# Optimization experiments

Hardware: AMD Instinct MI355X
Metric: run time of the kernel (lower is better)

Reference implementation:

```python
import jax, jax.numpy as jnp
import numpy as np

N, E, C = 50000, 800000, 100000
D_IN, HID = 128, 128
MLP_IN, MLP_HID = 2 * HID + 1, HID // 2
BN_EPS = 1e-5
NEG_SLOPE = 0.01


def setup_inputs() -> dict:
    key = jax.random.key(0)
    ks = jax.random.split(key, 24)
    inp = {
        "x": jax.random.normal(ks[0], (N, D_IN), jnp.float32),
        "src": jax.random.randint(ks[1], (E,), 0, N, jnp.int32),
        "dst": jax.random.randint(ks[2], (E,), 0, N, jnp.int32),
        "cand_u": jax.random.randint(ks[3], (C,), 0, N, jnp.int32),
        "cand_v": jax.random.randint(ks[4], (C,), 0, N, jnp.int32),
        "cand_feat": jax.random.normal(ks[5], (C, 1), jnp.float32),
    }
    s = 1.0 / np.sqrt(D_IN)
    # SAGEConv layer 0 and 1 (in=out=128 since statedim == pnhid)
    for li, k0 in [(0, 6), (1, 12)]:
        inp[f"w_self{li}"] = jax.random.uniform(ks[k0], (D_IN, HID), jnp.float32, -s, s)
        inp[f"w_neigh{li}"] = jax.random.uniform(ks[k0 + 1], (D_IN, HID), jnp.float32, -s, s)
        inp[f"b{li}"] = jnp.zeros((HID,), jnp.float32)
        inp[f"gamma{li}"] = jnp.ones((HID,), jnp.float32)
        inp[f"beta{li}"] = jnp.zeros((HID,), jnp.float32)
        inp[f"rm{li}"] = jax.random.normal(ks[k0 + 2], (HID,), jnp.float32) * 0.1
        inp[f"rv{li}"] = jax.random.uniform(ks[k0 + 3], (HID,), jnp.float32, 0.5, 1.5)
    # confidence MLP: 257 -> 64 -> 64 -> 1
    sizes = [MLP_IN, MLP_HID, MLP_HID, 1]
    for i in range(3):
        si = 1.0 / np.sqrt(sizes[i])
        inp[f"mw{i}"] = jax.random.uniform(ks[18 + 2 * i], (sizes[i], sizes[i + 1]), jnp.float32, -si, si)
        inp[f"mb{i}"] = jax.random.uniform(ks[19 + 2 * i], (sizes[i + 1],), jnp.float32, -si, si)
    return inp


def _sage_bn_block(x, src, dst, w_self, w_neigh, b, gamma, beta, rm, rv):
    # mean aggregation over incoming edges (gather -> scatter-add -> divide)
    msgs = x[src]  # [E, D]
    agg = jax.ops.segment_sum(msgs, dst, num_segments=N)  # [N, D]
    deg = jax.ops.segment_sum(jnp.ones((src.shape[0],), x.dtype), dst, num_segments=N)
    agg = agg / jnp.maximum(deg, 1.0)[:, None]
    h = x @ w_self + agg @ w_neigh + b
    # BatchNorm1d (eval mode, running stats) then leaky_relu; dropout is identity in eval
    h = gamma * (h - rm) * jax.lax.rsqrt(rv + BN_EPS) + beta
    return jax.nn.leaky_relu(h, NEG_SLOPE)


def reference(x, src, dst, cand_u, cand_v, cand_feat,
              w_self0, w_neigh0, b0, gamma0, beta0, rm0, rv0,
              w_self1, w_neigh1, b1, gamma1, beta1, rm1, rv1,
              mw0, mb0, mw1, mb1, mw2, mb2):
    h = _sage_bn_block(x, src, dst, w_self0, w_neigh0, b0, gamma0, beta0, rm0, rv0)
    h = _sage_bn_block(h, src, dst, w_self1, w_neigh1, b1, gamma1, beta1, rm1, rv1)
    h = jnp.nan_to_num(h, nan=1e-14)
    # candidate embeddings: [C, 2*HID + 1]
    ce = jnp.concatenate([h[cand_u], h[cand_v], cand_feat], axis=-1)
    z = jax.nn.leaky_relu(ce @ mw0 + mb0, NEG_SLOPE)
    z = jax.nn.leaky_relu(z @ mw1 + mb1, NEG_SLOPE)
    y = z @ mw2 + mb2  # [C, 1]
    return y, jax.nn.softmax(y, axis=0)
```

## Files before the change

kernel.cpp:

```cpp
#include <hip/hip_runtime.h>
#include <math.h>

#define N_NODES 50000
#define N_EDGES 800000
#define N_CAND  100000
#define D       128
#define BN_EPS  1e-5f
#define SLOPE   0.01f

#define NB2     196
#define TILE    4096
#define NTILE   196
#define BCAP    4736

typedef __attribute__((ext_vector_type(8))) short bf16x8;
typedef __attribute__((ext_vector_type(4))) float f32x4;

__device__ __forceinline__ float lrelu(float x){ return x >= 0.f ? x : SLOPE * x; }

__device__ __forceinline__ unsigned short f2bf_rn(float f){
  unsigned int u = __float_as_uint(f);
  unsigned int r = u + 0x7FFFu + ((u >> 16) & 1u);
  return (unsigned short)(r >> 16);
}
__device__ __forceinline__ float bf2f(unsigned short h){
  return __uint_as_float(((unsigned int)h) << 16);
}
__device__ __forceinline__ float4 bf4f(ushort4 u){
  return make_float4(__uint_as_float((unsigned)u.x << 16),
                     __uint_as_float((unsigned)u.y << 16),
                     __uint_as_float((unsigned)u.z << 16),
                     __uint_as_float((unsigned)u.w << 16));
}

__global__ __launch_bounds__(256) void k_bin(const int* __restrict__ src, const int* __restrict__ dst,
                                             int* __restrict__ gcnt, unsigned* __restrict__ ebin, int E){
  __shared__ unsigned stage[TILE];
  __shared__ int hist[256], lscan[256], lex[256], lcur[256], gbase[256];
  __shared__ int stot;
  int t = threadIdx.x;
  int e0 = blockIdx.x * TILE;

  hist[t] = 0;
  __syncthreads();

  unsigned pk[16]; int bk[16]; bool ok[16];
  #pragma unroll
  for (int j = 0; j < 16; ++j){
    int i = e0 + j * 256 + t;
    ok[j] = (i < E);
    if (ok[j]){
      int d = dst[i];
      pk[j] = ((unsigned)d << 16) | (unsigned)src[i];
      bk[j] = d >> 8;
      atomicAdd(&hist[bk[j]], 1);
    }
  }
  __syncthreads();

  lscan[t] = hist[t];
  __syncthreads();
  for (int off = 1; off < 256; off <<= 1){
    int v = (t >= off) ? lscan[t - off] : 0;
    __syncthreads();
    lscan[t] += v;
    __syncthreads();
  }
  int ex = lscan[t] - hist[t];
  lex[t]  = ex;
  lcur[t] = ex;
  if (t < NB2) gbase[t] = hist[t] ? atomicAdd(&gcnt[t], hist[t]) : 0;
  if (t == 255) stot = lscan[255];
  __syncthreads();

  #pragma unroll
  for (int j = 0; j < 16; ++j){
    if (ok[j]){
      int p = atomicAdd(&lcur[bk[j]], 1);
      stage[p] = pk[j];
    }
  }
  __syncthreads();

  int tot = stot;
  for (int i = t; i < tot; i += 256){
    unsigned e = stage[i];
    int b = (int)(e >> 24);
    ebin[(size_t)b * BCAP + gbase[b] + (i - lex[b])] = e;
  }
}

__global__ __launch_bounds__(256) void k_bscan2(const int* __restrict__ gcnt, int* __restrict__ bbase,
                                                int* __restrict__ rowptr){
  __shared__ int sd[256];
  int t = threadIdx.x;
  int v = (t < NB2) ? gcnt[t] : 0;
  sd[t] = v; __syncthreads();
  for (int off = 1; off < 256; off <<= 1){
    int a = (t >= off) ? sd[t - off] : 0;
    __syncthreads();
    sd[t] += a; __syncthreads();
  }
  if (t < NB2) bbase[t] = sd[t] - v;
  if (t == NB2 - 1) rowptr[N_NODES] = sd[t];
}

__global__ __launch_bounds__(256) void k_bfin(const int* __restrict__ gcnt, const int* __restrict__ bbase,
                                              const unsigned* __restrict__ ebin,
                                              unsigned short* __restrict__ eid16,
                                              int* __restrict__ rowptr, int n){
  __shared__ int hist[256], lb[256], lcur[256];
  int t = threadIdx.x, b = blockIdx.x;
  int cb   = gcnt[b];
  int base = bbase[b];
  const unsigned* eb = &ebin[(size_t)b * BCAP];
  hist[t] = 0;
  __syncthreads();
  for (int idx = t; idx < cb; idx += 256) atomicAdd(&hist[(eb[idx] >> 16) & 255], 1);
  __syncthreads();
  lb[t] = hist[t];
  __syncthreads();
  for (int off = 1; off < 256; off <<= 1){
    int v = (t >= off) ? lb[t - off] : 0;
    __syncthreads();
    lb[t] += v; __syncthreads();
  }
  int ex = lb[t] - hist[t];
  lcur[t] = ex;
  int node = (b << 8) + t;
  if (node < n) rowptr[node] = base + ex;
  __syncthreads();
  for (int idx = t; idx < cb; idx += 256){
    unsigned e = eb[idx];
    int p = atomicAdd(&lcur[(e >> 16) & 255], 1);
    eid16[base + p] = (unsigned short)(e & 0xffffu);
  }
}

__global__ __launch_bounds__(256) void k_cvt_w(const float* __restrict__ ws, const float* __restrict__ wn,
                                               unsigned short* __restrict__ bth, unsigned short* __restrict__ btl){
  int col = blockIdx.x;
  int k   = threadIdx.x;
  float v = (k < 128) ? ws[k * D + col] : wn[(k - 128) * D + col];
  unsigned short hi = f2bf_rn(v);
  unsigned short lo = f2bf_rn(v - bf2f(hi));
  bth[col * 256 + k] = hi;
  btl[col * 256 + k] = lo;
}

__global__ __launch_bounds__(256) void k_cvt_mlp(const float* __restrict__ w, int K, int Kpad,
                                                 unsigned short* __restrict__ th, unsigned short* __restrict__ tl){
  int col = blockIdx.x;
  for (int k = threadIdx.x; k < Kpad; k += 256){
    float v = (k < K) ? w[k * 64 + col] : 0.f;
    unsigned short hi = f2bf_rn(v);
    th[col * Kpad + k] = hi;
    tl[col * Kpad + k] = f2bf_rn(v - bf2f(hi));
  }
}

__global__ __launch_bounds__(256) void k_cvt_x(const float* __restrict__ X, unsigned short* __restrict__ XB, int nel4){
  int i = blockIdx.x * 256 + threadIdx.x;
  if (i < nel4){
    float4 v = *reinterpret_cast<const float4*>(&X[(size_t)i * 4]);
    ushort4 u;
    u.x = f2bf_rn(v.x); u.y = f2bf_rn(v.y); u.z = f2bf_rn(v.z); u.w = f2bf_rn(v.w);
    *reinterpret_cast<ushort4*>(&XB[(size_t)i * 4]) = u;
  }
}

__global__ __launch_bounds__(256) void k_agg_bf(const unsigned short* __restrict__ XB,
                                                const int* __restrict__ rowptr, const unsigned short* __restrict__ eid,
                                                float* __restrict__ AG, int n){
  int g = blockIdx.x * 8 + (threadIdx.x >> 5);
  int l = threadIdx.x & 31;
  if (g >= n) return;
  int e0 = rowptr[g], e1 = rowptr[g + 1];
  float4 a0 = make_float4(0.f,0.f,0.f,0.f);
  float4 a1 = make_float4(0.f,0.f,0.f,0.f);
  float4 a2 = make_float4(0.f,0.f,0.f,0.f);
  float4 a3 = make_float4(0.f,0.f,0.f,0.f);
  int e = e0;
  for (; e + 4 <= e1; e += 4){
    int s0 = eid[e], s1 = eid[e + 1], s2 = eid[e + 2], s3 = eid[e + 3];
    ushort4 u0 = *reinterpret_cast<const ushort4*>(&XB[(size_t)s0 * D + l * 4]);
    ushort4 u1 = *reinterpret_cast<const ushort4*>(&XB[(size_t)s1 * D + l * 4]);
    ushort4 u2 = *reinterpret_cast<const ushort4*>(&XB[(size_t)s2 * D + l * 4]);
    ushort4 u3 = *reinterpret_cast<const ushort4*>(&XB[(size_t)s3 * D + l * 4]);
    float4 f0 = bf4f(u0), f1 = bf4f(u1), f2 = bf4f(u2), f3 = bf4f(u3);
    a0.x += f0.x; a0.y += f0.y; a0.z += f0.z; a0.w += f0.w;
    a1.x += f1.x; a1.y += f1.y; a1.z += f1.z; a1.w += f1.w;
    a2.x += f2.x; a2.y += f2.y; a2.z += f2.z; a2.w += f2.w;
    a3.x += f3.x; a3.y += f3.y; a3.z += f3.z; a3.w += f3.w;
  }
  for (; e < e1; ++e){
    int s0 = eid[e];
    ushort4 u0 = *reinterpret_cast<const ushort4*>(&XB[(size_t)s0 * D + l * 4]);
    float4 f0 = bf4f(u0);
    a0.x += f0.x; a0.y += f0.y; a0.z += f0.z; a0.w += f0.w;
  }
  float sc = 1.f / fmaxf((float)(e1 - e0), 1.f);
  float4 o;
  o.x = (a0.x + a1.x + a2.x + a3.x) * sc;
  o.y = (a0.y + a1.y + a2.y + a3.y) * sc;
  o.z = (a0.z + a1.z + a2.z + a3.z) * sc;
  o.w = (a0.w + a1.w + a2.w + a3.w) * sc;
  *reinterpret_cast<float4*>(&AG[(size_t)g * D + l * 4]) = o;
}

__global__ __launch_bounds__(256) void k_sage_mfma(const float* __restrict__ XS, const float* __restrict__ AG,
    const unsigned short* __restrict__ BTH, const unsigned short* __restrict__ BTL,
    const float* __restrict__ Bb, const float* __restrict__ GM, const float* __restrict__ BT,
    const float* __restrict__ RM, const float* __restrict__ RV,
    float* __restrict__ H, unsigned short* __restrict__ HBH, unsigned short* __restrict__ HBL,
    int n, int donan)
{
  __shared__ unsigned short Ah[64 * 40];
  __shared__ unsigned short Al[64 * 40];
  __shared__ unsigned short Bh[128 * 40];
  __shared__ unsigned short Bl[128 * 40];

  int t  = threadIdx.x;
  int l  = t & 63;
  int wv = t >> 6;
  int lm = l & 15;
  int lk = l >> 4;
  int node0 = blockIdx.x * 64;

  f32x4 acc[8];
  #pragma unroll
  for (int f = 0; f < 8; ++f) acc[f] = (f32x4){0.f, 0.f, 0.f, 0.f};

  for (int step = 0; step < 8; ++step){
    int k0 = step * 32;
    const float* srcA = (step < 4) ? XS : AG;
    int koff = (step < 4) ? k0 : (k0 - 128);

    __syncthreads();
    #pragma unroll
    for (int i = 0; i < 2; ++i){
      int c   = t + i * 256;
      int row = c >> 3, c4 = c & 7;
      int node = min(node0 + row, n - 1);
      float4 v = *reinterpret_cast<const float4*>(&srcA[(size_t)node * D + koff + c4 * 4]);
      const float* vp = (const float*)&v;
      unsigned short hh[4], ll[4];
      #pragma unroll
      for (int j = 0; j < 4; ++j){
        unsigned short hi = f2bf_rn(vp[j]);
        hh[j] = hi;
        ll[j] = f2bf_rn(vp[j] - bf2f(hi));
      }
      uint2 wh, wl;
      wh.x = (unsigned)hh[0] | ((unsigned)hh[1] << 16);
      wh.y = (unsigned)hh[2] | ((unsigned)hh[3] << 16);
      wl.x = (unsigned)ll[0] | ((unsigned)ll[1] << 16);
      wl.y = (unsigned)ll[2] | ((unsigned)ll[3] << 16);
      *reinterpret_cast<uint2*>(&Ah[row * 40 + c4 * 4]) = wh;
      *reinterpret_cast<uint2*>(&Al[row * 40 + c4 * 4]) = wl;
    }
    #pragma unroll
    for (int i = 0; i < 2; ++i){
      int c   = t + i * 256;
      int col = c >> 2, q = c & 3;
      *reinterpret_cast<uint4*>(&Bh[col * 40 + q * 8]) =
          *reinterpret_cast<const uint4*>(&BTH[col * 256 + k0 + q * 8]);
      *reinterpret_cast<uint4*>(&Bl[col * 40 + q * 8]) =
          *reinterpret_cast<const uint4*>(&BTL[col * 256 + k0 + q * 8]);
    }
    __syncthreads();

    bf16x8 afh = *reinterpret_cast<const bf16x8*>(&Ah[(wv * 16 + lm) * 40 + lk * 8]);
    bf16x8 afl = *reinterpret_cast<const bf16x8*>(&Al[(wv * 16 + lm) * 40 + lk * 8]);
    #pragma unroll
    for (int f = 0; f < 8; ++f){
      bf16x8 bfh = *reinterpret_cast<const bf16x8*>(&Bh[(f * 16 + lm) * 40 + lk * 8]);
      bf16x8 bfl = *reinterpret_cast<const bf16x8*>(&Bl[(f * 16 + lm) * 40 + lk * 8]);
      acc[f] = __builtin_amdgcn_mfma_f32_16x16x32_bf16(afh, bfh, acc[f], 0, 0, 0);
      acc[f] = __builtin_amdgcn_mfma_f32_16x16x32_bf16(afl, bfh, acc[f], 0, 0, 0);
      acc[f] = __builtin_amdgcn_mfma_f32_16x16x32_bf16(afh, bfl, acc[f], 0, 0, 0);
    }
  }

  #pragma unroll
  for (int f = 0; f < 8; ++f){
    int col = f * 16 + lm;
    float s  = GM[col] * rsqrtf(RV[col] + BN_EPS);
    float cj = (Bb[col] - RM[col]) * s + BT[col];
    #pragma unroll
    for (int r = 0; r < 4; ++r){
      int node = node0 + wv * 16 + lk * 4 + r;
      if (node < n){
        float v = lrelu(acc[f][r] * s + cj);
        if (donan && (v != v)) v = 1e-14f;
        if (H)  H[(size_t)node * D + col] = v;
        unsigned short h16 = f2bf_rn(v);
        if (HBH) HBH[(size_t)node * D + col] = h16;
        if (HBL) HBL[(size_t)node * D + col] = f2bf_rn(v - bf2f(h16));
      }
    }
  }
}

__global__ __launch_bounds__(256) void k_mlp_mfma(
    const unsigned short* __restrict__ HH, const unsigned short* __restrict__ HL,
    const int* __restrict__ cu, const int* __restrict__ cv, const float* __restrict__ cf,
    const unsigned short* __restrict__ W0H, const unsigned short* __restrict__ W0L,
    const float* __restrict__ mw0, const float* __restrict__ mb0,
    const unsigned short* __restrict__ W1H, const unsigned short* __restrict__ W1L,
    const float* __restrict__ mb1, const float* __restrict__ mw2, const float* __restrict__ mb2,
    float* __restrict__ y, int C)
{
  __shared__ unsigned short zh[4][32 * 72];
  __shared__ unsigned short zl[4][32 * 72];

  int t = threadIdx.x;
  int wv = t >> 6, l = t & 63, lm = l & 15, lk = l >> 4;
  int candbase = blockIdx.x * 128 + wv * 32;

  int c0 = min(candbase + lm,      C - 1);
  int c1 = min(candbase + 16 + lm, C - 1);
  int nu0 = cu[c0], nv0 = cv[c0];
  int nu1 = cu[c1], nv1 = cv[c1];

  f32x4 acc[2][4];
  #pragma unroll
  for (int m = 0; m < 2; ++m)
    #pragma unroll
    for (int f = 0; f < 4; ++f) acc[m][f] = (f32x4){0.f, 0.f, 0.f, 0.f};

  int kbase = lk * 8;
  bf16x8 ah0 = *reinterpret_cast<const bf16x8*>(&HH[(size_t)nu0 * D + kbase]);
  bf16x8 al0 = *reinterpret_cast<const bf16x8*>(&HL[(size_t)nu0 * D + kbase]);
  bf16x8 ah1 = *reinterpret_cast<const bf16x8*>(&HH[(size_t)nu1 * D + kbase]);
  bf16x8 al1 = *reinterpret_cast<const bf16x8*>(&HL[(size_t)nu1 * D + kbase]);

  #pragma unroll
  for (int s = 0; s < 8; ++s){
    bf16x8 nh0, nl0, nh1, nl1;
    if (s < 7){
      int n0 = (s + 1 < 4) ? nu0 : nv0;
      int n1 = (s + 1 < 4) ? nu1 : nv1;
      int koff = ((s + 1) & 3) * 32 + kbase;
      nh0 = *reinterpret_cast<const bf16x8*>(&HH[(size_t)n0 * D + koff]);
      nl0 = *reinterpret_cast<const bf16x8*>(&HL[(size_t)n0 * D + koff]);
      nh1 = *reinterpret_cast<const bf16x8*>(&HH[(size_t)n1 * D + koff]);
      nl1 = *reinterpret_cast<const bf16x8*>(&HL[(size_t)n1 * D + koff]);
    }
    int k0 = s * 32 + kbase;
    #pragma unroll
    for (int f = 0; f < 4; ++f){
      int col = f * 16 + lm;
      bf16x8 bh = *reinterpret_cast<const bf16x8*>(&W0H[(size_t)col * 264 + k0]);
      bf16x8 bl = *reinterpret_cast<const bf16x8*>(&W0L[(size_t)col * 264 + k0]);
      acc[0][f] = __builtin_amdgcn_mfma_f32_16x16x32_bf16(ah0, bh, acc[0][f], 0, 0, 0);
      acc[0][f] = __builtin_amdgcn_mfma_f32_16x16x32_bf16(al0, bh, acc[0][f], 0, 0, 0);
      acc[0][f] = __builtin_amdgcn_mfma_f32_16x16x32_bf16(ah0, bl, acc[0][f], 0, 0, 0);
      acc[1][f] = __builtin_amdgcn_mfma_f32_16x16x32_bf16(ah1, bh, acc[1][f], 0, 0, 0);
      acc[1][f] = __builtin_amdgcn_mfma_f32_16x16x32_bf16(al1, bh, acc[1][f], 0, 0, 0);
      acc[1][f] = __builtin_amdgcn_mfma_f32_16x16x32_bf16(ah1, bl, acc[1][f], 0, 0, 0);
    }
    if (s < 7){ ah0 = nh0; al0 = nl0; ah1 = nh1; al1 = nl1; }
  }

  float cfv[2][4];
  #pragma unroll
  for (int m = 0; m < 2; ++m)
    #pragma unroll
    for (int r = 0; r < 4; ++r)
      cfv[m][r] = cf[min(candbase + m * 16 + lk * 4 + r, C - 1)];

  #pragma unroll
  for (int f = 0; f < 4; ++f){
    int col = f * 16 + lm;
    float b0v = mb0[col];
    float wfv = mw0[256 * 64 + col];
    #pragma unroll
    for (int m = 0; m < 2; ++m){
      #pragma unroll
      for (int r = 0; r < 4; ++r){
        int cl = m * 16 + lk * 4 + r;
        float z = lrelu(acc[m][f][r] + b0v + cfv[m][r] * wfv);
        unsigned short h16 = f2bf_rn(z);
        zh[wv][cl * 72 + col] = h16;
        zl[wv][cl * 72 + col] = f2bf_rn(z - bf2f(h16));
      }
    }
  }

  f32x4 a2[2][4];
  #pragma unroll
  for (int m = 0; m < 2; ++m)
    #pragma unroll
    for (int f = 0; f < 4; ++f) a2[m][f] = (f32x4){0.f, 0.f, 0.f, 0.f};

  #pragma unroll
  for (int s2 = 0; s2 < 2; ++s2){
    int kk = s2 * 32 + kbase;
    bf16x8 azh0 = *reinterpret_cast<const bf16x8*>(&zh[wv][(0 * 16 + lm) * 72 + kk]);
    bf16x8 azl0 = *reinterpret_cast<const bf16x8*>(&zl[wv][(0 * 16 + lm) * 72 + kk]);
    bf16x8 azh1 = *reinterpret_cast<const bf16x8*>(&zh[wv][(1 * 16 + lm) * 72 + kk]);
    bf16x8 azl1 = *reinterpret_cast<const bf16x8*>(&zl[wv][(1 * 16 + lm) * 72 + kk]);
    #pragma unroll
    for (int f = 0; f < 4; ++f){
      int col = f * 16 + lm;
      bf16x8 bh = *reinterpret_cast<const bf16x8*>(&W1H[(size_t)col * 64 + kk]);
      bf16x8 bl = *reinterpret_cast<const bf16x8*>(&W1L[(size_t)col * 64 + kk]);
      a2[0][f] = __builtin_amdgcn_mfma_f32_16x16x32_bf16(azh0, bh, a2[0][f], 0, 0, 0);
      a2[0][f] = __builtin_amdgcn_mfma_f32_16x16x32_bf16(azl0, bh, a2[0][f], 0, 0, 0);
      a2[0][f] = __builtin_amdgcn_mfma_f32_16x16x32_bf16(azh0, bl, a2[0][f], 0, 0, 0);
      a2[1][f] = __builtin_amdgcn_mfma_f32_16x16x32_bf16(azh1, bh, a2[1][f], 0, 0, 0);
      a2[1][f] = __builtin_amdgcn_mfma_f32_16x16x32_bf16(azl1, bh, a2[1][f], 0, 0, 0);
      a2[1][f] = __builtin_amdgcn_mfma_f32_16x16x32_bf16(azh1, bl, a2[1][f], 0, 0, 0);
    }
  }

  float p00 = 0.f, p01 = 0.f, p02 = 0.f, p03 = 0.f;
  float p10 = 0.f, p11 = 0.f, p12 = 0.f, p13 = 0.f;
  #pragma unroll
  for (int f = 0; f < 4; ++f){
    int col = f * 16 + lm;
    float b1v = mb1[col];
    float w2v = mw2[col];
    p00 = fmaf(lrelu(a2[0][f][0] + b1v), w2v, p00);
    p01 = fmaf(lrelu(a2[0][f][1] + b1v), w2v, p01);
    p02 = fmaf(lrelu(a2[0][f][2] + b1v), w2v, p02);
    p03 = fmaf(lrelu(a2[0][f][3] + b1v), w2v, p03);
    p10 = fmaf(lrelu(a2[1][f][0] + b1v), w2v, p10);
    p11 = fmaf(lrelu(a2[1][f][1] + b1v), w2v, p11);
    p12 = fmaf(lrelu(a2[1][f][2] + b1v), w2v, p12);
    p13 = fmaf(lrelu(a2[1][f][3] + b1v), w2v, p13);
  }
  #pragma unroll
  for (int off = 1; off < 16; off <<= 1){
    p00 += __shfl_xor(p00, off); p01 += __shfl_xor(p01, off);
    p02 += __shfl_xor(p02, off); p03 += __shfl_xor(p03, off);
    p10 += __shfl_xor(p10, off); p11 += __shfl_xor(p11, off);
    p12 += __shfl_xor(p12, off); p13 += __shfl_xor(p13, off);
  }
  if (lm == 0){
    float b2 = mb2[0];
    int base0 = candbase + lk * 4;
    int base1 = candbase + 16 + lk * 4;
    if (base0 + 0 < C) y[base0 + 0] = p00 + b2;
    if (base0 + 1 < C) y[base0 + 1] = p01 + b2;
    if (base0 + 2 < C) y[base0 + 2] = p02 + b2;
    if (base0 + 3 < C) y[base0 + 3] = p03 + b2;
    if (base1 + 0 < C) y[base1 + 0] = p10 + b2;
    if (base1 + 1 < C) y[base1 + 1] = p11 + b2;
    if (base1 + 2 < C) y[base1 + 2] = p12 + b2;
    if (base1 + 3 < C) y[base1 + 3] = p13 + b2;
  }
}

__global__ __launch_bounds__(256) void k_red1(const float* __restrict__ y,
                                              float* __restrict__ bmax, float* __restrict__ bsum, int C){
  __shared__ float sm[4];
  __shared__ float ss[4];
  int t = threadIdx.x;
  float m = -3.4e38f;
  for (int i = blockIdx.x * 256 + t; i < C; i += gridDim.x * 256) m = fmaxf(m, y[i]);
  for (int o = 32; o; o >>= 1) m = fmaxf(m, __shfl_xor(m, o));
  if ((t & 63) == 0) sm[t >> 6] = m;
  __syncthreads();
  float bm = fmaxf(fmaxf(sm[0], sm[1]), fmaxf(sm[2], sm[3]));
  float s = 0.f;
  for (int i = blockIdx.x * 256 + t; i < C; i += gridDim.x * 256) s += expf(y[i] - bm);
  for (int o = 32; o; o >>= 1) s += __shfl_xor(s, o);
  if ((t & 63) == 0) ss[t >> 6] = s;
  __syncthreads();
  if (t == 0){ bmax[blockIdx.x] = bm; bsum[blockIdx.x] = ss[0] + ss[1] + ss[2] + ss[3]; }
}

__global__ __launch_bounds__(256) void k_red2(const float* __restrict__ bmax, const float* __restrict__ bsum,
                                              float* __restrict__ g, int nb){
  __shared__ float sm[4];
  __shared__ float ss[4];
  int t = threadIdx.x;
  float m0 = (t < nb) ? bmax[t] : -3.4e38f;
  float m = m0;
  for (int o = 32; o; o >>= 1) m = fmaxf(m, __shfl_xor(m, o));
  if ((t & 63) == 0) sm[t >> 6] = m;
  __syncthreads();
  float gm = fmaxf(fmaxf(sm[0], sm[1]), fmaxf(sm[2], sm[3]));
  float s = (t < nb) ? bsum[t] * expf(m0 - gm) : 0.f;
  for (int o = 32; o; o >>= 1) s += __shfl_xor(s, o);
  if ((t & 63) == 0) ss[t >> 6] = s;
  __syncthreads();
  if (t == 0){ g[0] = gm; g[1] = 1.f / (ss[0] + ss[1] + ss[2] + ss[3]); }
}

__global__ __launch_bounds__(256) void k_red3(const float* __restrict__ y, const float* __restrict__ g,
                                              float* __restrict__ out, int C){
  int i = blockIdx.x * 256 + threadIdx.x;
  if (i < C) out[i] = expf(y[i] - g[0]) * g[1];
}

extern "C" void kernel_launch(void* const* d_in, const int* in_sizes, int n_in,
                              void* d_out, int out_size, void* d_ws, size_t ws_size,
                              hipStream_t stream)
{
  const float* x   = (const float*)d_in[0];
  const int*   src = (const int*)  d_in[1];
  const int*   dst = (const int*)  d_in[2];
  const int*   cu  = (const int*)  d_in[3];
  const int*   cv  = (const int*)  d_in[4];
  const float* cf  = (const float*)d_in[5];
  const float* ws0 = (const float*)d_in[6];
  const float* wn0 = (const float*)d_in[7];
  const float* b0  = (const float*)d_in[8];
  const float* g0  = (const float*)d_in[9];
  const float* be0 = (const float*)d_in[10];
  const float* rm0 = (const float*)d_in[11];
  const float* rv0 = (const float*)d_in[12];
  const float* ws1 = (const float*)d_in[13];
  const float* wn1 = (const float*)d_in[14];
  const float* b1  = (const float*)d_in[15];
  const float* g1  = (const float*)d_in[16];
  const float* be1 = (const float*)d_in[17];
  const float* rm1 = (const float*)d_in[18];
  const float* rv1 = (const float*)d_in[19];
  const float* mw0 = (const float*)d_in[20];
  const float* mb0 = (const float*)d_in[21];
  const float* mw1 = (const float*)d_in[22];
  const float* mb1 = (const float*)d_in[23];
  const float* mw2 = (const float*)d_in[24];
  const float* mb2 = (const float*)d_in[25];

  float* out = (float*)d_out;

  char* w = (char*)d_ws;
  float* aggn  = (float*)w; w += (size_t)N_NODES * D * 4;
  float* h0    = (float*)w; w += (size_t)N_NODES * D * 4;
  float* h1    = (float*)w; w += (size_t)N_NODES * D * 4;
  int* cnt     = (int*)w;   w += (size_t)N_NODES * 4;
  int* rowptr  = (int*)w;   w += (size_t)(N_NODES + 1) * 4;
  int* cur     = (int*)w;   w += (size_t)N_NODES * 4;
  int* eid     = (int*)w;   w += (size_t)N_EDGES * 4;
  int* gcnt    = (int*)w;   w += (size_t)(NB2 + 8) * 4;
  int* bbase   = (int*)w;   w += (size_t)(NB2 + 1) * 4;
  float* bmax  = (float*)w; w += 256 * 4;
  float* bsumF = (float*)w; w += 256 * 4;
  float* gred  = (float*)w; w += 2 * 4;
  unsigned short* w0th = (unsigned short*)w; w += (size_t)64 * 264 * 2;
  unsigned short* w0tl = (unsigned short*)w; w += (size_t)64 * 264 * 2;
  unsigned short* w1th = (unsigned short*)w; w += (size_t)64 * 64 * 2;
  unsigned short* w1tl = (unsigned short*)w; w += (size_t)64 * 64 * 2;

  unsigned short* eid16 = (unsigned short*)eid;

  unsigned* ebin = (unsigned*)h0;

  unsigned short* xb   = (unsigned short*)h1;
  unsigned short* hb0  = xb + (size_t)N_NODES * D;
  unsigned short* hb1h = (unsigned short*)h1;
  unsigned short* hb1l = hb1h + (size_t)N_NODES * D;

  unsigned short* bth0 = (unsigned short*)cnt;
  unsigned short* btl0 = bth0 + 128 * 256;
  unsigned short* bth1 = (unsigned short*)cur;
  unsigned short* btl1 = bth1 + 128 * 256;

  hipMemsetAsync(gcnt, 0, (size_t)NB2 * 4, stream);
  k_bin   <<<NTILE, 256, 0, stream>>>(src, dst, gcnt, ebin, N_EDGES);
  k_bscan2<<<1, 256, 0, stream>>>(gcnt, bbase, rowptr);
  k_bfin  <<<NB2, 256, 0, stream>>>(gcnt, bbase, ebin, eid16, rowptr, N_NODES);

  k_cvt_w<<<128, 256, 0, stream>>>(ws0, wn0, bth0, btl0);
  k_cvt_w<<<128, 256, 0, stream>>>(ws1, wn1, bth1, btl1);
  k_cvt_mlp<<<64, 256, 0, stream>>>(mw0, 257, 264, w0th, w0tl);
  k_cvt_mlp<<<64, 256, 0, stream>>>(mw1, 64, 64, w1th, w1tl);
  k_cvt_x<<<(N_NODES * D / 4 + 255) / 256, 256, 0, stream>>>(x, xb, N_NODES * D / 4);

  int GB = (N_NODES + 63) / 64;
  k_agg_bf<<<(N_NODES + 7) / 8, 256, 0, stream>>>(xb, rowptr, eid16, aggn, N_NODES);
  k_sage_mfma<<<GB, 256, 0, stream>>>(x,  aggn, bth0, btl0, b0, g0, be0, rm0, rv0,
                                      h0, hb0, (unsigned short*)0, N_NODES, 0);
  k_agg_bf<<<(N_NODES + 7) / 8, 256, 0, stream>>>(hb0, rowptr, eid16, aggn, N_NODES);
  k_sage_mfma<<<GB, 256, 0, stream>>>(h0, aggn, bth1, btl1, b1, g1, be1, rm1, rv1,
                                      (float*)0, hb1h, hb1l, N_NODES, 1);

  k_mlp_mfma<<<(N_CAND + 127) / 128, 256, 0, stream>>>(hb1h, hb1l, cu, cv, cf,
      w0th, w0tl, mw0, mb0, w1th, w1tl, mb1, mw2, mb2, out, N_CAND);

  k_red1<<<256, 256, 0, stream>>>(out, bmax, bsumF, N_CAND);
  k_red2<<<1, 256, 0, stream>>>(bmax, bsumF, gred, 256);
  k_red3<<<(N_CAND + 255) / 256, 256, 0, stream>>>(out, gred, out + N_CAND, N_CAND);
}
```

Baseline: 230.2 us.

## Precompute per-node first MLP layer projections instead of per-candidate GEMM

The first MLP layer is linear in the concatenated node embeddings, so it is split into per-node projections h@W_u and h@W_v, computed once for all 50k nodes by a new GEMM kernel and stored as hi/lo bf16 pairs. The candidate kernel then gathers two 64-wide projected rows per candidate and adds them with bias and the scalar feature term, replacing the 257-deep per-candidate MFMA. This roughly halves the layer-0 FLOPs (50k vs 100k rows) but adds a separate kernel launch and an extra write and read of the projected buffers. Storing the projections as split bf16 adds a small rounding step before the sum.

```diff
diff --git a/kernel.cpp b/kernel.cpp
--- a/kernel.cpp
+++ b/kernel.cpp
@@ -26,11 +26,25 @@
 __device__ __forceinline__ float bf2f(unsigned short h){
   return __uint_as_float(((unsigned int)h) << 16);
 }
+__device__ __forceinline__ float bfu(unsigned u){ return __uint_as_float(u << 16); }
+__device__ __forceinline__ float bfh(unsigned u){ return __uint_as_float(u & 0xffff0000u); }
 __device__ __forceinline__ float4 bf4f(ushort4 u){
   return make_float4(__uint_as_float((unsigned)u.x << 16),
                      __uint_as_float((unsigned)u.y << 16),
                      __uint_as_float((unsigned)u.z << 16),
                      __uint_as_float((unsigned)u.w << 16));
+}
+
+__device__ __forceinline__ unsigned pk_bf16(float a, float b){
+  unsigned r;
+  asm("v_cvt_pk_bf16_f32 %0, %1, %2" : "=v"(r) : "v"(a), "v"(b));
+  return r;
+}
+__device__ __forceinline__ void split2(float a, float b, unsigned &h, unsigned &l){
+  h = pk_bf16(a, b);
+  float ra = a - __uint_as_float(h << 16);
+  float rb = b - __uint_as_float(h & 0xffff0000u);
+  l = pk_bf16(ra, rb);
 }
 
 __global__ __launch_bounds__(256) void k_bin(const int* __restrict__ src, const int* __restrict__ dst,
@@ -157,6 +171,16 @@
     th[col * Kpad + k] = hi;
     tl[col * Kpad + k] = f2bf_rn(v - bf2f(hi));
   }
+}
+
+__global__ __launch_bounds__(128) void k_cvt_w0cat(const float* __restrict__ mw0,
+                                                   unsigned short* __restrict__ ch, unsigned short* __restrict__ cl_){
+  int col = blockIdx.x;
+  int k   = threadIdx.x;
+  float v = (col < 64) ? mw0[k * 64 + col] : mw0[(128 + k) * 64 + (col - 64)];
+  unsigned short hi = f2bf_rn(v);
+  ch [col * 128 + k] = hi;
+  cl_[col * 128 + k] = f2bf_rn(v - bf2f(hi));
 }
 
 __global__ __launch_bounds__(256) void k_cvt_x(const float* __restrict__ X, unsigned short* __restrict__ XB, int nel4){
@@ -302,10 +326,88 @@
   }
 }
 
-__global__ __launch_bounds__(256) void k_mlp_mfma(
+__global__ __launch_bounds__(256) void k_pgemm(
     const unsigned short* __restrict__ HH, const unsigned short* __restrict__ HL,
+    const unsigned short* __restrict__ WCH, const unsigned short* __restrict__ WCL,
+    unsigned short* __restrict__ PH, unsigned short* __restrict__ PL, int n)
+{
+  __shared__ unsigned short Ah[64 * 40];
+  __shared__ unsigned short Al[64 * 40];
+  __shared__ unsigned short Bh[128 * 40];
+  __shared__ unsigned short Bl[128 * 40];
+
+  int t  = threadIdx.x;
+  int l  = t & 63;
+  int wv = t >> 6;
+  int lm = l & 15;
+  int lk = l >> 4;
+  int node0 = blockIdx.x * 64;
+
+  f32x4 acc[8];
+  #pragma unroll
+  for (int f = 0; f < 8; ++f) acc[f] = (f32x4){0.f, 0.f, 0.f, 0.f};
+
+  for (int step = 0; step < 4; ++step){
+    int k0 = step * 32;
+    __syncthreads();
+    {
+      int row = t >> 2, q = t & 3;
+      int node = min(node0 + row, n - 1);
+      *reinterpret_cast<uint4*>(&Ah[row * 40 + q * 8]) =
+          *reinterpret_cast<const uint4*>(&HH[(size_t)node * D + k0 + q * 8]);
+      *reinterpret_cast<uint4*>(&Al[row * 40 + q * 8]) =
+          *reinterpret_cast<const uint4*>(&HL[(size_t)node * D + k0 + q * 8]);
+    }
+    #pragma unroll
+    for (int i = 0; i < 2; ++i){
+      int c = t + i * 256;
+      int col = c >> 2, q = c & 3;
+      *reinterpret_cast<uint4*>(&Bh[col * 40 + q * 8]) =
+          *reinterpret_cast<const uint4*>(&WCH[col * 128 + k0 + q * 8]);
+      *reinterpret_cast<uint4*>(&Bl[col * 40 + q * 8]) =
+          *reinterpret_cast<const uint4*>(&WCL[col * 128 + k0 + q * 8]);
+    }
+    __syncthreads();
+
+    bf16x8 afh = *reinterpret_cast<const bf16x8*>(&Ah[(wv * 16 + lm) * 40 + lk * 8]);
+    bf16x8 afl = *reinterpret_cast<const bf16x8*>(&Al[(wv * 16 + lm) * 40 + lk * 8]);
+    #pragma unroll
+    for (int f = 0; f < 8; ++f){
+      bf16x8 bfh = *reinterpret_cast<const bf16x8*>(&Bh[(f * 16 + lm) * 40 + lk * 8]);
+      bf16x8 bfl = *reinterpret_cast<const bf16x8*>(&Bl[(f * 16 + lm) * 40 + lk * 8]);
+      acc[f] = __builtin_amdgcn_mfma_f32_16x16x32_bf16(afh, bfh, acc[f], 0, 0, 0);
+      acc[f] = __builtin_amdgcn_mfma_f32_16x16x32_bf16(afl, bfh, acc[f], 0, 0, 0);
+      acc[f] = __builtin_amdgcn_mfma_f32_16x16x32_bf16(afh, bfl, acc[f], 0, 0, 0);
+    }
+  }
+
+  #pragma unroll
+  for (int f = 0; f < 8; ++f){
+    int col = f * 16 + lm;
+    #pragma unroll
+    for (int r = 0; r < 4; ++r){
+      int node = node0 + wv * 16 + lk * 4 + r;
+      if (node < n){
+        float v = acc[f][r];
+        unsigned short h16 = f2bf_rn(v);
+        PH[(size_t)node * D + col] = h16;
+        PL[(size_t)node * D + col] = f2bf_rn(v - bf2f(h16));
+      }
+    }
+  }
+}
+
+__device__ __forceinline__ void proc2(unsigned uh, unsigned ul, unsigned vh, unsigned vl,
+                                      float wfa, float wfb, float b0a, float b0b, float cfv,
+                                      unsigned &ho, unsigned &lo_){
+  float z0 = lrelu(bfu(uh) + bfu(ul) + bfu(vh) + bfu(vl) + cfv * wfa + b0a);
+  float z1 = lrelu(bfh(uh) + bfh(ul) + bfh(vh) + bfh(vl) + cfv * wfb + b0b);
+  split2(z0, z1, ho, lo_);
+}
+
+__global__ __launch_bounds__(256) void k_mlp2(
+    const unsigned short* __restrict__ PH, const unsigned short* __restrict__ PL,
     const int* __restrict__ cu, const int* __restrict__ cv, const float* __restrict__ cf,
-    const unsigned short* __restrict__ W0H, const unsigned short* __restrict__ W0L,
     const float* __restrict__ mw0, const float* __restrict__ mb0,
     const unsigned short* __restrict__ W1H, const unsigned short* __restrict__ W1L,
     const float* __restrict__ mb1, const float* __restrict__ mw2, const float* __restrict__ mb2,
@@ -313,81 +415,48 @@
 {
   __shared__ unsigned short zh[4][32 * 72];
   __shared__ unsigned short zl[4][32 * 72];
+  __shared__ float bw[64], ww[64];
 
   int t = threadIdx.x;
   int wv = t >> 6, l = t & 63, lm = l & 15, lk = l >> 4;
+  int cl = l & 31, hsel = l >> 5;
   int candbase = blockIdx.x * 128 + wv * 32;
 
-  int c0 = min(candbase + lm,      C - 1);
-  int c1 = min(candbase + 16 + lm, C - 1);
-  int nu0 = cu[c0], nv0 = cv[c0];
-  int nu1 = cu[c1], nv1 = cv[c1];
-
-  f32x4 acc[2][4];
-  #pragma unroll
-  for (int m = 0; m < 2; ++m)
-    #pragma unroll
-    for (int f = 0; f < 4; ++f) acc[m][f] = (f32x4){0.f, 0.f, 0.f, 0.f};
+  if (t < 64){ bw[t] = mb0[t]; ww[t] = mw0[256 * 64 + t]; }
+  __syncthreads();
+
+  int cc = min(candbase + cl, C - 1);
+  int nu = cu[cc], nv = cv[cc];
+  float cfv = cf[cc];
+
+  const uint4* puh = reinterpret_cast<const uint4*>(&PH[(size_t)nu * D + hsel * 32]);
+  const uint4* pul = reinterpret_cast<const uint4*>(&PL[(size_t)nu * D + hsel * 32]);
+  const uint4* pvh = reinterpret_cast<const uint4*>(&PH[(size_t)nv * D + 64 + hsel * 32]);
+  const uint4* pvl = reinterpret_cast<const uint4*>(&PL[(size_t)nv * D + 64 + hsel * 32]);
+  uint4 uh0 = puh[0], uh1 = puh[1], uh2 = puh[2], uh3 = puh[3];
+  uint4 ul0 = pul[0], ul1 = pul[1], ul2 = pul[2], ul3 = pul[3];
+  uint4 vh0 = pvh[0], vh1 = pvh[1], vh2 = pvh[2], vh3 = pvh[3];
+  uint4 vl0 = pvl[0], vl1 = pvl[1], vl2 = pvl[2], vl3 = pvl[3];
+
+  int colb = hsel * 32;
+  unsigned short* zhr = &zh[wv][cl * 72];
+  unsigned short* zlr = &zl[wv][cl * 72];
+  #define PROC_W(UH, UL, VH, VL, CO) { \
+    unsigned ho, lo_; \
+    proc2(UH, UL, VH, VL, ww[colb + (CO)], ww[colb + (CO) + 1], bw[colb + (CO)], bw[colb + (CO) + 1], cfv, ho, lo_); \
+    *reinterpret_cast<unsigned*>(&zhr[colb + (CO)]) = ho; \
+    *reinterpret_cast<unsigned*>(&zlr[colb + (CO)]) = lo_; }
+  PROC_W(uh0.x, ul0.x, vh0.x, vl0.x, 0)  PROC_W(uh0.y, ul0.y, vh0.y, vl0.y, 2)
+  PROC_W(uh0.z, ul0.z, vh0.z, vl0.z, 4)  PROC_W(uh0.w, ul0.w, vh0.w, vl0.w, 6)
+  PROC_W(uh1.x, ul1.x, vh1.x, vl1.x, 8)  PROC_W(uh1.y, ul1.y, vh1.y, vl1.y, 10)
+  PROC_W(uh1.z, ul1.z, vh1.z, vl1.z, 12) PROC_W(uh1.w, ul1.w, vh1.w, vl1.w, 14)
+  PROC_W(uh2.x, ul2.x, vh2.x, vl2.x, 16) PROC_W(uh2.y, ul2.y, vh2.y, vl2.y, 18)
+  PROC_W(uh2.z, ul2.z, vh2.z, vl2.z, 20) PROC_W(uh2.w, ul2.w, vh2.w, vl2.w, 22)
+  PROC_W(uh3.x, ul3.x, vh3.x, vl3.x, 24) PROC_W(uh3.y, ul3.y, vh3.y, vl3.y, 26)
+  PROC_W(uh3.z, ul3.z, vh3.z, vl3.z, 28) PROC_W(uh3.w, ul3.w, vh3.w, vl3.w, 30)
+  #undef PROC_W
 
   int kbase = lk * 8;
-  bf16x8 ah0 = *reinterpret_cast<const bf16x8*>(&HH[(size_t)nu0 * D + kbase]);
-  bf16x8 al0 = *reinterpret_cast<const bf16x8*>(&HL[(size_t)nu0 * D + kbase]);
-  bf16x8 ah1 = *reinterpret_cast<const bf16x8*>(&HH[(size_t)nu1 * D + kbase]);
-  bf16x8 al1 = *reinterpret_cast<const bf16x8*>(&HL[(size_t)nu1 * D + kbase]);
-
-  #pragma unroll
-  for (int s = 0; s < 8; ++s){
-    bf16x8 nh0, nl0, nh1, nl1;
-    if (s < 7){
-      int n0 = (s + 1 < 4) ? nu0 : nv0;
-      int n1 = (s + 1 < 4) ? nu1 : nv1;
-      int koff = ((s + 1) & 3) * 32 + kbase;
-      nh0 = *reinterpret_cast<const bf16x8*>(&HH[(size_t)n0 * D + koff]);
-      nl0 = *reinterpret_cast<const bf16x8*>(&HL[(size_t)n0 * D + koff]);
-      nh1 = *reinterpret_cast<const bf16x8*>(&HH[(size_t)n1 * D + koff]);
-      nl1 = *reinterpret_cast<const bf16x8*>(&HL[(size_t)n1 * D + koff]);
-    }
-    int k0 = s * 32 + kbase;
-    #pragma unroll
-    for (int f = 0; f < 4; ++f){
-      int col = f * 16 + lm;
-      bf16x8 bh = *reinterpret_cast<const bf16x8*>(&W0H[(size_t)col * 264 + k0]);
-      bf16x8 bl = *reinterpret_cast<const bf16x8*>(&W0L[(size_t)col * 264 + k0]);
-      acc[0][f] = __builtin_amdgcn_mfma_f32_16x16x32_bf16(ah0, bh, acc[0][f], 0, 0, 0);
-      acc[0][f] = __builtin_amdgcn_mfma_f32_16x16x32_bf16(al0, bh, acc[0][f], 0, 0, 0);
-      acc[0][f] = __builtin_amdgcn_mfma_f32_16x16x32_bf16(ah0, bl, acc[0][f], 0, 0, 0);
-      acc[1][f] = __builtin_amdgcn_mfma_f32_16x16x32_bf16(ah1, bh, acc[1][f], 0, 0, 0);
-      acc[1][f] = __builtin_amdgcn_mfma_f32_16x16x32_bf16(al1, bh, acc[1][f], 0, 0, 0);
-      acc[1][f] = __builtin_amdgcn_mfma_f32_16x16x32_bf16(ah1, bl, acc[1][f], 0, 0, 0);
-    }
-    if (s < 7){ ah0 = nh0; al0 = nl0; ah1 = nh1; al1 = nl1; }
-  }
-
-  float cfv[2][4];
-  #pragma unroll
-  for (int m = 0; m < 2; ++m)
-    #pragma unroll
-    for (int r = 0; r < 4; ++r)
-      cfv[m][r] = cf[min(candbase + m * 16 + lk * 4 + r, C - 1)];
-
-  #pragma unroll
-  for (int f = 0; f < 4; ++f){
-    int col = f * 16 + lm;
-    float b0v = mb0[col];
-    float wfv = mw0[256 * 64 + col];
-    #pragma unroll
-    for (int m = 0; m < 2; ++m){
-      #pragma unroll
-      for (int r = 0; r < 4; ++r){
-        int cl = m * 16 + lk * 4 + r;
-        float z = lrelu(acc[m][f][r] + b0v + cfv[m][r] * wfv);
-        unsigned short h16 = f2bf_rn(z);
-        zh[wv][cl * 72 + col] = h16;
-        zl[wv][cl * 72 + col] = f2bf_rn(z - bf2f(h16));
-      }
-    }
-  }
-
   f32x4 a2[2][4];
   #pragma unroll
   for (int m = 0; m < 2; ++m)
@@ -542,10 +611,10 @@
   float* bmax  = (float*)w; w += 256 * 4;
   float* bsumF = (float*)w; w += 256 * 4;
   float* gred  = (float*)w; w += 2 * 4;
-  unsigned short* w0th = (unsigned short*)w; w += (size_t)64 * 264 * 2;
-  unsigned short* w0tl = (unsigned short*)w; w += (size_t)64 * 264 * 2;
-  unsigned short* w1th = (unsigned short*)w; w += (size_t)64 * 64 * 2;
-  unsigned short* w1tl = (unsigned short*)w; w += (size_t)64 * 64 * 2;
+  unsigned short* w1th  = (unsigned short*)w; w += (size_t)64 * 64 * 2;
+  unsigned short* w1tl  = (unsigned short*)w; w += (size_t)64 * 64 * 2;
+  unsigned short* w0cth = (unsigned short*)w; w += (size_t)128 * 128 * 2;
+  unsigned short* w0ctl = (unsigned short*)w; w += (size_t)128 * 128 * 2;
 
   unsigned short* eid16 = (unsigned short*)eid;
 
@@ -556,6 +625,9 @@
   unsigned short* hb1h = (unsigned short*)h1;
   unsigned short* hb1l = hb1h + (size_t)N_NODES * D;
 
+  unsigned short* pbh = (unsigned short*)aggn;
+  unsigned short* pbl = pbh + (size_t)N_NODES * D;
+
   unsigned short* bth0 = (unsigned short*)cnt;
   unsigned short* btl0 = bth0 + 128 * 256;
   unsigned short* bth1 = (unsigned short*)cur;
@@ -568,8 +640,8 @@
 
   k_cvt_w<<<128, 256, 0, stream>>>(ws0, wn0, bth0, btl0);
   k_cvt_w<<<128, 256, 0, stream>>>(ws1, wn1, bth1, btl1);
-  k_cvt_mlp<<<64, 256, 0, stream>>>(mw0, 257, 264, w0th, w0tl);
   k_cvt_mlp<<<64, 256, 0, stream>>>(mw1, 64, 64, w1th, w1tl);
+  k_cvt_w0cat<<<128, 128, 0, stream>>>(mw0, w0cth, w0ctl);
   k_cvt_x<<<(N_NODES * D / 4 + 255) / 256, 256, 0, stream>>>(x, xb, N_NODES * D / 4);
 
   int GB = (N_NODES + 63) / 64;
@@ -580,8 +652,10 @@
   k_sage_mfma<<<GB, 256, 0, stream>>>(h0, aggn, bth1, btl1, b1, g1, be1, rm1, rv1,
                                       (float*)0, hb1h, hb1l, N_NODES, 1);
 
-  k_mlp_mfma<<<(N_CAND + 127) / 128, 256, 0, stream>>>(hb1h, hb1l, cu, cv, cf,
-      w0th, w0tl, mw0, mb0, w1th, w1tl, mb1, mw2, mb2, out, N_CAND);
+  k_pgemm<<<GB, 256, 0, stream>>>(hb1h, hb1l, w0cth, w0ctl, pbh, pbl, N_NODES);
+
+  k_mlp2<<<(N_CAND + 127) / 128, 256, 0, stream>>>(pbh, pbl, cu, cv, cf,
+      mw0, mb0, w1th, w1tl, mb1, mw2, mb2, out, N_CAND);
 
   k_red1<<<256, 256, 0, stream>>>(out, bmax, bsumF, N_CAND);
   k_red2<<<1, 256, 0, stream>>>(bmax, bsumF, gred, 256);
```

New measurement: 227.6 us. About the same (-1.1%).
